# Optimization experiments

Measured on AMD Instinct MI355X. Metric: run time of the kernel, lower is better.

The kernel has to match this reference:

```python
import jax, jax.numpy as jnp
import numpy as np

N = 50000
H = 256
EPS = 1e-5

def setup_inputs() -> dict:
    key = jax.random.key(0)
    ks = jax.random.split(key, 8)
    d = 128
    inp = {
        'x': jax.random.normal(ks[0], (N, d), jnp.float32),
        'edge_index': jax.random.randint(ks[1], (2, 800000), 0, N, jnp.int64),
        'W1': jax.random.normal(ks[2], (d, H), jnp.float32) * (2.0 / d) ** 0.5,
        'b1': jnp.zeros((H,), jnp.float32),
        'g1': jnp.ones((H,), jnp.float32),
        'be1': jnp.zeros((H,), jnp.float32),
        'W2': jax.random.normal(ks[3], (H, H), jnp.float32) * (2.0 / H) ** 0.5,
        'b2': jnp.zeros((H,), jnp.float32),
        'g2': jnp.ones((H,), jnp.float32),
        'be2': jnp.zeros((H,), jnp.float32),
        'W3': jax.random.normal(ks[4], (H, H), jnp.float32) * (2.0 / H) ** 0.5,
        'b3': jnp.zeros((H,), jnp.float32),
        'g3': jnp.ones((H,), jnp.float32),
        'be3': jnp.zeros((H,), jnp.float32),
        'Wf1': jax.random.normal(ks[5], (H, H // 2), jnp.float32) * (2.0 / H) ** 0.5,
        'bf1': jnp.zeros((H // 2,), jnp.float32),
        'Wf2': jax.random.normal(ks[6], (H // 2, 1), jnp.float32) * (2.0 / (H // 2)) ** 0.5,
        'bf2': jnp.zeros((1,), jnp.float32),
    }
    return inp

def _gcn_norm(edge_index):
    # add self-loops, symmetric normalization (PyG GCNConv defaults)
    loop = jnp.arange(N, dtype=edge_index.dtype)
    row = jnp.concatenate([edge_index[0], loop])  # source
    col = jnp.concatenate([edge_index[1], loop])  # target
    deg = jax.ops.segment_sum(jnp.ones_like(col, jnp.float32), col, num_segments=N)
    dis = jnp.where(deg > 0, jax.lax.rsqrt(deg), 0.0)
    norm = dis[row] * dis[col]  # [E+N]
    return row, col, norm

def _conv(x, W, b, row, col, norm):
    xw = x @ W                       # [N,H]
    msg = xw[row] * norm[:, None]    # gather + scale, [E+N,H]
    out = jax.ops.segment_sum(msg, col, num_segments=N)
    return out + b

def _ln(x, g, b):
    mu = jnp.mean(x, axis=-1, keepdims=True)
    var = jnp.var(x, axis=-1, keepdims=True)
    return (x - mu) * jax.lax.rsqrt(var + EPS) * g + b

def reference(x, edge_index, W1, b1, g1, be1, W2, b2, g2, be2, W3, b3, g3, be3, Wf1, bf1, Wf2, bf2):
    row, col, norm = _gcn_norm(edge_index)
    x1 = jax.nn.relu(_ln(_conv(x, W1, b1, row, col, norm), g1, be1))
    x2 = jax.nn.relu(_ln(_conv(x1, W2, b2, row, col, norm), g2, be2)) + 0.7 * x1
    x3 = jax.nn.relu(_ln(_conv(x2, W3, b3, row, col, norm), g3, be3)) * 0.7 + x2
    h = jax.nn.relu(x3 @ Wf1 + bf1)
    return h @ Wf2 + bf2  # [N,1]
```

## Files before the change

kernel.cpp:

```cpp
#include <hip/hip_runtime.h>
#include <cstdint>
#include <cstddef>

#define HDIM 256
#define DIN 128
#define EPSV 1e-5f
#define SCHUNK 1024

typedef __attribute__((ext_vector_type(8))) short short8;
typedef __attribute__((ext_vector_type(4))) float f32x4;

__device__ __forceinline__ float bf2f(unsigned int u16) {
  union { unsigned int i; float f; } v; v.i = u16 << 16; return v.f;
}
__device__ __forceinline__ unsigned short f2bf(float f) {
  union { float f; unsigned int i; } v; v.f = f;
  unsigned int u = v.i;
  return (unsigned short)((u + 0x7fffu + ((u >> 16) & 1u)) >> 16);
}
__device__ __forceinline__ float4 ldbf4(const unsigned short* p) {
  uint2 v = *(const uint2*)p;
  return make_float4(bf2f(v.x & 0xffffu), bf2f(v.x >> 16),
                     bf2f(v.y & 0xffffu), bf2f(v.y >> 16));
}
__device__ __forceinline__ void stbf4(unsigned short* p, float a, float b, float c, float d) {
  uint2 o;
  o.x = (unsigned int)f2bf(a) | ((unsigned int)f2bf(b) << 16);
  o.y = (unsigned int)f2bf(c) | ((unsigned int)f2bf(d) << 16);
  *(uint2*)p = o;
}
#define ACC8(u) do { \
    acc[0] += bf2f((u).x & 0xffffu); acc[1] += bf2f((u).x >> 16); \
    acc[2] += bf2f((u).y & 0xffffu); acc[3] += bf2f((u).y >> 16); \
    acc[4] += bf2f((u).z & 0xffffu); acc[5] += bf2f((u).z >> 16); \
    acc[6] += bf2f((u).w & 0xffffu); acc[7] += bf2f((u).w >> 16); } while (0)

__global__ __launch_bounds__(256) void zero_i_k(int* deg, int* cur, int n) {
  int i = blockIdx.x * 256 + threadIdx.x;
  if (i < n) { deg[i] = 0; cur[i] = 0; }
}

__global__ __launch_bounds__(256) void hist_k(const int* __restrict__ col, int* deg, int e) {
  int i = blockIdx.x * 256 + threadIdx.x;
  if (i < e) atomicAdd(&deg[col[i]], 1);
}

__global__ __launch_bounds__(256) void scanA_k(const int* __restrict__ deg,
                                               int* __restrict__ row_ptr,
                                               int* __restrict__ blockSums,
                                               float* __restrict__ dis, int n) {
  __shared__ int waveSums[4];
  const int tid = threadIdx.x, lane = tid & 63, w = tid >> 6;
  const int base = blockIdx.x * SCHUNK + tid * 4;
  int v0 = 0, v1 = 0, v2 = 0, v3 = 0;
  if (base + 0 < n) v0 = deg[base + 0];
  if (base + 1 < n) v1 = deg[base + 1];
  if (base + 2 < n) v2 = deg[base + 2];
  if (base + 3 < n) v3 = deg[base + 3];
  if (base + 0 < n) dis[base + 0] = rsqrtf((float)(v0 + 1));
  if (base + 1 < n) dis[base + 1] = rsqrtf((float)(v1 + 1));
  if (base + 2 < n) dis[base + 2] = rsqrtf((float)(v2 + 1));
  if (base + 3 < n) dis[base + 3] = rsqrtf((float)(v3 + 1));
  int tsum = v0 + v1 + v2 + v3;
  int inc = tsum;
#pragma unroll
  for (int off = 1; off < 64; off <<= 1) {
    int t = __shfl_up(inc, off);
    if (lane >= off) inc += t;
  }
  if (lane == 63) waveSums[w] = inc;
  __syncthreads();
  int woff = 0;
#pragma unroll
  for (int k = 0; k < 4; ++k) woff += (k < w) ? waveSums[k] : 0;
  int excl = woff + inc - tsum;
  if (base + 0 < n) row_ptr[base + 0] = excl;
  if (base + 1 < n) row_ptr[base + 1] = excl + v0;
  if (base + 2 < n) row_ptr[base + 2] = excl + v0 + v1;
  if (base + 3 < n) row_ptr[base + 3] = excl + v0 + v1 + v2;
  if (tid == 255) blockSums[blockIdx.x] = woff + inc;
}

__global__ __launch_bounds__(256) void scanB_k(int* blockSums, int nb) {
  __shared__ int waveSums[4];
  const int tid = threadIdx.x, lane = tid & 63, w = tid >> 6;
  int v = (tid < nb) ? blockSums[tid] : 0;
  int inc = v;
#pragma unroll
  for (int off = 1; off < 64; off <<= 1) {
    int t = __shfl_up(inc, off);
    if (lane >= off) inc += t;
  }
  if (lane == 63) waveSums[w] = inc;
  __syncthreads();
  int woff = 0;
#pragma unroll
  for (int k = 0; k < 4; ++k) woff += (k < w) ? waveSums[k] : 0;
  if (tid < nb) blockSums[tid] = woff + inc - v;
}

__global__ __launch_bounds__(256) void scanC_k(int* __restrict__ row_ptr,
                                               const int* __restrict__ blockSums,
                                               int n, int e) {
  const int base = blockIdx.x * SCHUNK + threadIdx.x * 4;
  const int add = blockSums[blockIdx.x];
#pragma unroll
  for (int k = 0; k < 4; ++k)
    if (base + k < n) row_ptr[base + k] += add;
  if (blockIdx.x == 0 && threadIdx.x == 0) row_ptr[n] = e;
}

__global__ __launch_bounds__(256) void fill_k(const int* __restrict__ row,
                                              const int* __restrict__ col,
                                              const int* __restrict__ row_ptr,
                                              int* cur, int* srcs, int e) {
  int i = blockIdx.x * 256 + threadIdx.x;
  if (i < e) {
    int c = col[i];
    int p = row_ptr[c] + atomicAdd(&cur[c], 1);
    srcs[p] = row[i];
  }
}

__device__ __forceinline__ void packW(const float* __restrict__ W,
                                      unsigned short* __restrict__ out,
                                      int idx, int C) {
  int j = idx & 7, lane = (idx >> 3) & 63, rest = idx >> 9;
  int NSUB = C >> 4;
  int ns = rest % NSUB, kb = rest / NSUB;
  int k = kb * 32 + (lane >> 4) * 8 + j;
  int c = ns * 16 + (lane & 15);
  out[idx] = f2bf(W[(size_t)k * C + c]);
}

__global__ __launch_bounds__(256) void prep_k(
    const float* __restrict__ W1, const float* __restrict__ W2,
    const float* __restrict__ W3, const float* __restrict__ Wf1,
    const float* __restrict__ x, const float* __restrict__ dis,
    unsigned short* __restrict__ W1p, unsigned short* __restrict__ W2p,
    unsigned short* __restrict__ W3p, unsigned short* __restrict__ Wf1p,
    unsigned short* __restrict__ xs, int nx) {
  int idx = blockIdx.x * 256 + threadIdx.x;
  const int s0 = DIN * HDIM, s1 = s0 + HDIM * HDIM, s2 = s1 + HDIM * HDIM,
            s3 = s2 + HDIM * 128;
  if (idx < s0) packW(W1, W1p, idx, HDIM);
  else if (idx < s1) packW(W2, W2p, idx - s0, HDIM);
  else if (idx < s2) packW(W3, W3p, idx - s1, HDIM);
  else if (idx < s3) packW(Wf1, Wf1p, idx - s2, 128);
  else {
    int o = idx - s3;
    if (o < nx) xs[o] = f2bf(x[o] * dis[o >> 7]);
  }
}

__global__ __launch_bounds__(256) void gather256_k(
    const unsigned short* __restrict__ xs, const int* __restrict__ row_ptr,
    const int* __restrict__ srcs, const float* __restrict__ dis,
    unsigned short* __restrict__ out, int n) {
  int wv = blockIdx.x * 4 + (threadIdx.x >> 6);
  int lane = threadIdx.x & 63;
  int half = lane >> 5, li = lane & 31;
  int i = wv * 2 + half;
  bool valid = i < n;
  int ic = valid ? i : n - 1;
  int beg = row_ptr[ic], end = row_ptr[ic + 1];
  float di = dis[ic];
  const int co = li * 8;
  const unsigned short* xb = xs + co;
  float acc[8];
  {
    uint4 v = *(const uint4*)(xb + (size_t)ic * 256);
    acc[0] = bf2f(v.x & 0xffffu); acc[1] = bf2f(v.x >> 16);
    acc[2] = bf2f(v.y & 0xffffu); acc[3] = bf2f(v.y >> 16);
    acc[4] = bf2f(v.z & 0xffffu); acc[5] = bf2f(v.z >> 16);
    acc[6] = bf2f(v.w & 0xffffu); acc[7] = bf2f(v.w >> 16);
  }
  int j = beg;
  int4 sA, sB;
  if (j + 8 <= end) { sA = *(const int4*)(srcs + j); sB = *(const int4*)(srcs + j + 4); }
  for (; j + 8 <= end;) {
    int4 cA = sA, cB = sB;
    j += 8;
    if (j + 8 <= end) { sA = *(const int4*)(srcs + j); sB = *(const int4*)(srcs + j + 4); }
    uint4 u0 = *(const uint4*)(xb + (size_t)cA.x * 256);
    uint4 u1 = *(const uint4*)(xb + (size_t)cA.y * 256);
    uint4 u2 = *(const uint4*)(xb + (size_t)cA.z * 256);
    uint4 u3 = *(const uint4*)(xb + (size_t)cA.w * 256);
    uint4 u4 = *(const uint4*)(xb + (size_t)cB.x * 256);
    uint4 u5 = *(const uint4*)(xb + (size_t)cB.y * 256);
    uint4 u6 = *(const uint4*)(xb + (size_t)cB.z * 256);
    uint4 u7 = *(const uint4*)(xb + (size_t)cB.w * 256);
    ACC8(u0); ACC8(u1); ACC8(u2); ACC8(u3);
    ACC8(u4); ACC8(u5); ACC8(u6); ACC8(u7);
  }
  for (; j < end; ++j) {
    uint4 u = *(const uint4*)(xb + (size_t)srcs[j] * 256);
    ACC8(u);
  }
  if (valid) {
    uint4 o;
    o.x = (unsigned int)f2bf(di * acc[0]) | ((unsigned int)f2bf(di * acc[1]) << 16);
    o.y = (unsigned int)f2bf(di * acc[2]) | ((unsigned int)f2bf(di * acc[3]) << 16);
    o.z = (unsigned int)f2bf(di * acc[4]) | ((unsigned int)f2bf(di * acc[5]) << 16);
    o.w = (unsigned int)f2bf(di * acc[6]) | ((unsigned int)f2bf(di * acc[7]) << 16);
    *(uint4*)(out + (size_t)i * 256 + co) = o;
  }
}

__global__ __launch_bounds__(256) void gather128_k(
    const unsigned short* __restrict__ xs, const int* __restrict__ row_ptr,
    const int* __restrict__ srcs, const float* __restrict__ dis,
    unsigned short* __restrict__ out, int n) {
  int wv = blockIdx.x * 4 + (threadIdx.x >> 6);
  int lane = threadIdx.x & 63;
  int q = lane >> 4, li = lane & 15;
  int i = wv * 4 + q;
  bool valid = i < n;
  int ic = valid ? i : n - 1;
  int beg = row_ptr[ic], end = row_ptr[ic + 1];
  float di = dis[ic];
  const int co = li * 8;
  const unsigned short* xb = xs + co;
  float acc[8];
  {
    uint4 v = *(const uint4*)(xb + (size_t)ic * 128);
    acc[0] = bf2f(v.x & 0xffffu); acc[1] = bf2f(v.x >> 16);
    acc[2] = bf2f(v.y & 0xffffu); acc[3] = bf2f(v.y >> 16);
    acc[4] = bf2f(v.z & 0xffffu); acc[5] = bf2f(v.z >> 16);
    acc[6] = bf2f(v.w & 0xffffu); acc[7] = bf2f(v.w >> 16);
  }
  int j = beg;
  int4 sA, sB;
  if (j + 8 <= end) { sA = *(const int4*)(srcs + j); sB = *(const int4*)(srcs + j + 4); }
  for (; j + 8 <= end;) {
    int4 cA = sA, cB = sB;
    j += 8;
    if (j + 8 <= end) { sA = *(const int4*)(srcs + j); sB = *(const int4*)(srcs + j + 4); }
    uint4 u0 = *(const uint4*)(xb + (size_t)cA.x * 128);
    uint4 u1 = *(const uint4*)(xb + (size_t)cA.y * 128);
    uint4 u2 = *(const uint4*)(xb + (size_t)cA.z * 128);
    uint4 u3 = *(const uint4*)(xb + (size_t)cA.w * 128);
    uint4 u4 = *(const uint4*)(xb + (size_t)cB.x * 128);
    uint4 u5 = *(const uint4*)(xb + (size_t)cB.y * 128);
    uint4 u6 = *(const uint4*)(xb + (size_t)cB.z * 128);
    uint4 u7 = *(const uint4*)(xb + (size_t)cB.w * 128);
    ACC8(u0); ACC8(u1); ACC8(u2); ACC8(u3);
    ACC8(u4); ACC8(u5); ACC8(u6); ACC8(u7);
  }
  for (; j < end; ++j) {
    uint4 u = *(const uint4*)(xb + (size_t)srcs[j] * 128);
    ACC8(u);
  }
  if (valid) {
    uint4 o;
    o.x = (unsigned int)f2bf(di * acc[0]) | ((unsigned int)f2bf(di * acc[1]) << 16);
    o.y = (unsigned int)f2bf(di * acc[2]) | ((unsigned int)f2bf(di * acc[3]) << 16);
    o.z = (unsigned int)f2bf(di * acc[4]) | ((unsigned int)f2bf(di * acc[5]) << 16);
    o.w = (unsigned int)f2bf(di * acc[6]) | ((unsigned int)f2bf(di * acc[7]) << 16);
    *(uint4*)(out + (size_t)i * 128 + co) = o;
  }
}

template<int MODE, int K>
__global__ __launch_bounds__(512) void gemmln_k(
    const unsigned short* __restrict__ A, const unsigned short* __restrict__ Wp,
    const float* __restrict__ bias, const float* __restrict__ gam,
    const float* __restrict__ bet, const unsigned short* __restrict__ xprev,
    const float* __restrict__ dis, unsigned short* __restrict__ out,
    unsigned short* __restrict__ outs, int n) {
  constexpr int CN = 256, NSUB = 16, KC = K / 32;
  __shared__ float red_s[64][4], red_q[64][4];
  const int t = threadIdx.x;
  const int w = t >> 6, lane = t & 63;
  const int rg = w & 1, cg = w >> 1;
  const int gq = lane >> 4, i = lane & 15;
  const int m0 = blockIdx.x * 64;
  const int r0 = m0 + rg * 32 + i, r1 = r0 + 16;
  const int l0 = r0 < n ? r0 : n - 1, l1 = r1 < n ? r1 : n - 1;
  const unsigned short* a0 = A + (size_t)l0 * K + gq * 8;
  const unsigned short* a1 = A + (size_t)l1 * K + gq * 8;
  const short8* wp = (const short8*)Wp + (size_t)(cg * 4) * 64 + lane;

  f32x4 acc[2][4];
#pragma unroll
  for (int rr = 0; rr < 2; ++rr)
#pragma unroll
    for (int j = 0; j < 4; ++j) acc[rr][j] = (f32x4){0.f, 0.f, 0.f, 0.f};

  short8 af0 = *(const short8*)a0;
  short8 af1 = *(const short8*)a1;
  short8 wf[4];
#pragma unroll
  for (int j = 0; j < 4; ++j) wf[j] = wp[j * 64];

#pragma unroll
  for (int kc = 0; kc < KC; ++kc) {
    short8 naf0, naf1, nwf[4];
    if (kc + 1 < KC) {
      naf0 = *(const short8*)(a0 + (kc + 1) * 32);
      naf1 = *(const short8*)(a1 + (kc + 1) * 32);
#pragma unroll
      for (int j = 0; j < 4; ++j) nwf[j] = wp[(size_t)(kc + 1) * NSUB * 64 + j * 64];
    }
#pragma unroll
    for (int j = 0; j < 4; ++j) {
      acc[0][j] = __builtin_amdgcn_mfma_f32_16x16x32_bf16(wf[j], af0, acc[0][j], 0, 0, 0);
      acc[1][j] = __builtin_amdgcn_mfma_f32_16x16x32_bf16(wf[j], af1, acc[1][j], 0, 0, 0);
    }
    if (kc + 1 < KC) {
      af0 = naf0; af1 = naf1;
#pragma unroll
      for (int j = 0; j < 4; ++j) wf[j] = nwf[j];
    }
  }

  const int colb = cg * 64 + gq * 4;
  float s0 = 0.f, q0 = 0.f, s1 = 0.f, q1 = 0.f;
#pragma unroll
  for (int j = 0; j < 4; ++j) {
    f32x4 b4 = *(const f32x4*)(bias + colb + j * 16);
#pragma unroll
    for (int r = 0; r < 4; ++r) {
      acc[0][j][r] += b4[r];
      acc[1][j][r] += b4[r];
      float v = acc[0][j][r]; s0 += v; q0 += v * v;
      float u = acc[1][j][r]; s1 += u; q1 += u * u;
    }
  }
  s0 += __shfl_xor(s0, 16); s0 += __shfl_xor(s0, 32);
  q0 += __shfl_xor(q0, 16); q0 += __shfl_xor(q0, 32);
  s1 += __shfl_xor(s1, 16); s1 += __shfl_xor(s1, 32);
  q1 += __shfl_xor(q1, 16); q1 += __shfl_xor(q1, 32);
  if (gq == 0) {
    red_s[rg * 32 + i][cg] = s0;      red_q[rg * 32 + i][cg] = q0;
    red_s[rg * 32 + 16 + i][cg] = s1; red_q[rg * 32 + 16 + i][cg] = q1;
  }
  __syncthreads();

#pragma unroll
  for (int rr = 0; rr < 2; ++rr) {
    int il = rg * 32 + rr * 16 + i;
    int r = m0 + il;
    if (r >= n) continue;
    float ss = (red_s[il][0] + red_s[il][1]) + (red_s[il][2] + red_s[il][3]);
    float qq = (red_q[il][0] + red_q[il][1]) + (red_q[il][2] + red_q[il][3]);
    float mu = ss * (1.f / CN);
    float inv = rsqrtf(qq * (1.f / CN) - mu * mu + EPSV);
    float sdi = outs ? dis[r] : 0.f;
    unsigned short* op = out + (size_t)r * CN + colb;
    unsigned short* osp = outs ? outs + (size_t)r * CN + colb : nullptr;
    const unsigned short* pp = (MODE != 0) ? (xprev + (size_t)r * CN + colb) : nullptr;
#pragma unroll
    for (int j = 0; j < 4; ++j) {
      f32x4 g4 = *(const f32x4*)(gam + colb + j * 16);
      f32x4 e4 = *(const f32x4*)(bet + colb + j * 16);
      float o0 = fmaxf((acc[rr][j][0] - mu) * inv * g4[0] + e4[0], 0.f);
      float o1 = fmaxf((acc[rr][j][1] - mu) * inv * g4[1] + e4[1], 0.f);
      float o2 = fmaxf((acc[rr][j][2] - mu) * inv * g4[2] + e4[2], 0.f);
      float o3 = fmaxf((acc[rr][j][3] - mu) * inv * g4[3] + e4[3], 0.f);
      if (MODE == 1) {
        float4 pv = ldbf4(pp + j * 16);
        o0 += 0.7f * pv.x; o1 += 0.7f * pv.y; o2 += 0.7f * pv.z; o3 += 0.7f * pv.w;
      } else if (MODE == 2) {
        float4 pv = ldbf4(pp + j * 16);
        o0 = o0 * 0.7f + pv.x; o1 = o1 * 0.7f + pv.y;
        o2 = o2 * 0.7f + pv.z; o3 = o3 * 0.7f + pv.w;
      }
      stbf4(op + j * 16, o0, o1, o2, o3);
      if (outs) stbf4(osp + j * 16, o0 * sdi, o1 * sdi, o2 * sdi, o3 * sdi);
    }
  }
}

__global__ __launch_bounds__(256) void gemmdot_k(
    const unsigned short* __restrict__ A, const unsigned short* __restrict__ Wp,
    const float* __restrict__ b1, const float* __restrict__ w2,
    const float* __restrict__ b2, float* __restrict__ out, int n) {
  constexpr int K = 256, NSUB = 8, KC = 8;
  __shared__ float redh[64][2];
  const int t = threadIdx.x;
  const int w = t >> 6, lane = t & 63;
  const int rg = w & 1, cg = w >> 1;
  const int gq = lane >> 4, i = lane & 15;
  const int m0 = blockIdx.x * 64;
  const int r0 = m0 + rg * 32 + i, r1 = r0 + 16;
  const int l0 = r0 < n ? r0 : n - 1, l1 = r1 < n ? r1 : n - 1;
  const unsigned short* a0 = A + (size_t)l0 * K + gq * 8;
  const unsigned short* a1 = A + (size_t)l1 * K + gq * 8;
  const short8* wp = (const short8*)Wp + (size_t)(cg * 4) * 64 + lane;

  f32x4 acc[2][4];
#pragma unroll
  for (int rr = 0; rr < 2; ++rr)
#pragma unroll
    for (int j = 0; j < 4; ++j) acc[rr][j] = (f32x4){0.f, 0.f, 0.f, 0.f};

  short8 af0 = *(const short8*)a0;
  short8 af1 = *(const short8*)a1;
  short8 wf[4];
#pragma unroll
  for (int j = 0; j < 4; ++j) wf[j] = wp[j * 64];

#pragma unroll
  for (int kc = 0; kc < KC; ++kc) {
    short8 naf0, naf1, nwf[4];
    if (kc + 1 < KC) {
      naf0 = *(const short8*)(a0 + (kc + 1) * 32);
      naf1 = *(const short8*)(a1 + (kc + 1) * 32);
#pragma unroll
      for (int j = 0; j < 4; ++j) nwf[j] = wp[(size_t)(kc + 1) * NSUB * 64 + j * 64];
    }
#pragma unroll
    for (int j = 0; j < 4; ++j) {
      acc[0][j] = __builtin_amdgcn_mfma_f32_16x16x32_bf16(wf[j], af0, acc[0][j], 0, 0, 0);
      acc[1][j] = __builtin_amdgcn_mfma_f32_16x16x32_bf16(wf[j], af1, acc[1][j], 0, 0, 0);
    }
    if (kc + 1 < KC) {
      af0 = naf0; af1 = naf1;
#pragma unroll
      for (int j = 0; j < 4; ++j) wf[j] = nwf[j];
    }
  }

  const int colb = cg * 64 + gq * 4;
  float p0 = 0.f, p1 = 0.f;
#pragma unroll
  for (int j = 0; j < 4; ++j) {
    f32x4 bb = *(const f32x4*)(b1 + colb + j * 16);
    f32x4 ww = *(const f32x4*)(w2 + colb + j * 16);
#pragma unroll
    for (int r = 0; r < 4; ++r) {
      p0 += fmaxf(acc[0][j][r] + bb[r], 0.f) * ww[r];
      p1 += fmaxf(acc[1][j][r] + bb[r], 0.f) * ww[r];
    }
  }
  p0 += __shfl_xor(p0, 16); p0 += __shfl_xor(p0, 32);
  p1 += __shfl_xor(p1, 16); p1 += __shfl_xor(p1, 32);
  if (gq == 0) {
    redh[rg * 32 + i][cg] = p0;
    redh[rg * 32 + 16 + i][cg] = p1;
  }
  __syncthreads();
  if (t < 64) {
    int r = m0 + t;
    if (r < n) out[r] = redh[t][0] + redh[t][1] + b2[0];
  }
}

extern "C" void kernel_launch(void* const* d_in, const int* in_sizes, int n_in,
                              void* d_out, int out_size, void* d_ws, size_t ws_size,
                              hipStream_t stream) {
  const float* x   = (const float*)d_in[0];
  const int*   ei  = (const int*)d_in[1];
  const float* W1  = (const float*)d_in[2];
  const float* b1  = (const float*)d_in[3];
  const float* g1  = (const float*)d_in[4];
  const float* be1 = (const float*)d_in[5];
  const float* W2  = (const float*)d_in[6];
  const float* b2  = (const float*)d_in[7];
  const float* g2  = (const float*)d_in[8];
  const float* be2 = (const float*)d_in[9];
  const float* W3  = (const float*)d_in[10];
  const float* b3  = (const float*)d_in[11];
  const float* g3  = (const float*)d_in[12];
  const float* be3 = (const float*)d_in[13];
  const float* Wf1 = (const float*)d_in[14];
  const float* bf1 = (const float*)d_in[15];
  const float* Wf2 = (const float*)d_in[16];
  const float* bf2 = (const float*)d_in[17];
  float* out = (float*)d_out;

  const int n = in_sizes[0] / DIN;
  const int e = in_sizes[1] / 2;
  const int* row = ei;
  const int* col = ei + e;

  char* ws = (char*)d_ws;
  size_t off = 0;
  auto alloc = [&](size_t bytes) -> void* {
    void* p = ws + off;
    off = (off + bytes + 255) & ~(size_t)255;
    return p;
  };
  float*          dis     = (float*)alloc((size_t)n * 4);
  int*            deg_i   = (int*)alloc((size_t)n * 4);
  int*            cur     = (int*)alloc((size_t)n * 4);
  int*            row_ptr = (int*)alloc((size_t)(n + 1) * 4);
  int*            bsums   = (int*)alloc((size_t)256 * 4);
  int*            srcs    = (int*)alloc((size_t)e * 4);
  unsigned short* W1p     = (unsigned short*)alloc((size_t)DIN * HDIM * 2);
  unsigned short* W2p     = (unsigned short*)alloc((size_t)HDIM * HDIM * 2);
  unsigned short* W3p     = (unsigned short*)alloc((size_t)HDIM * HDIM * 2);
  unsigned short* Wf1p    = (unsigned short*)alloc((size_t)HDIM * 128 * 2);
  unsigned short* xsb     = (unsigned short*)alloc((size_t)n * DIN * 2);
  unsigned short* agg     = (unsigned short*)alloc((size_t)n * HDIM * 2);
  unsigned short* x1      = (unsigned short*)alloc((size_t)n * HDIM * 2);
  unsigned short* x1s     = (unsigned short*)alloc((size_t)n * HDIM * 2);
  unsigned short* x2      = (unsigned short*)alloc((size_t)n * HDIM * 2);
  unsigned short* x2s     = (unsigned short*)alloc((size_t)n * HDIM * 2);
  unsigned short* a1      = agg;
  unsigned short* x3      = x1;

  const int nb  = (n + 255) / 256;
  const int eb  = (e + 255) / 256;
  const int gb  = (n + 63) / 64;
  const int sb_ = (n + SCHUNK - 1) / SCHUNK;
  const int g2b = (n + 7) / 8;
  const int g1b = (n + 15) / 16;
  const int prep_tot = DIN * HDIM + HDIM * HDIM + HDIM * HDIM + HDIM * 128 + n * DIN;

  zero_i_k<<<nb, 256, 0, stream>>>(deg_i, cur, n);
  hist_k<<<eb, 256, 0, stream>>>(col, deg_i, e);
  scanA_k<<<sb_, 256, 0, stream>>>(deg_i, row_ptr, bsums, dis, n);
  scanB_k<<<1, 256, 0, stream>>>(bsums, sb_);
  scanC_k<<<sb_, 256, 0, stream>>>(row_ptr, bsums, n, e);
  fill_k<<<eb, 256, 0, stream>>>(row, col, row_ptr, cur, srcs, e);

  prep_k<<<(prep_tot + 255) / 256, 256, 0, stream>>>(W1, W2, W3, Wf1, x, dis,
                                                     W1p, W2p, W3p, Wf1p, xsb, n * DIN);

  gather128_k<<<g1b, 256, 0, stream>>>(xsb, row_ptr, srcs, dis, a1, n);
  gemmln_k<0, DIN><<<gb, 512, 0, stream>>>(a1, W1p, b1, g1, be1, nullptr, dis, x1, x1s, n);

  gather256_k<<<g2b, 256, 0, stream>>>(x1s, row_ptr, srcs, dis, agg, n);
  gemmln_k<1, HDIM><<<gb, 512, 0, stream>>>(agg, W2p, b2, g2, be2, x1, dis, x2, x2s, n);

  gather256_k<<<g2b, 256, 0, stream>>>(x2s, row_ptr, srcs, dis, agg, n);
  gemmln_k<2, HDIM><<<gb, 512, 0, stream>>>(agg, W3p, b3, g3, be3, x2, dis, x3, nullptr, n);

  gemmdot_k<<<gb, 256, 0, stream>>>(x3, Wf1p, bf1, Wf2, bf2, out, n);
}
```

Baseline: 484.6 us.

## Store only scaled activations, merge scan passes, widen gather unroll, memset counters

The layer-norm GEMMs now write only the dis-scaled activation and recover the unscaled residual by multiplying with 1/dis. This drops one full N×256 bf16 store per layer and the separate residual buffers. The block-sum scan kernel is folded into scanC, where each block reduces its preceding block sums. The zeroing kernel is replaced by a single hipMemsetAsync. The gather loops issue 16 independent row loads per iteration instead of software-pipelining 8. The residual path now takes an extra bf16 rounding and a division by dis, which adds a small accuracy risk.

```diff
diff --git a/kernel.cpp b/kernel.cpp
--- a/kernel.cpp
+++ b/kernel.cpp
@@ -34,11 +34,6 @@
     acc[2] += bf2f((u).y & 0xffffu); acc[3] += bf2f((u).y >> 16); \
     acc[4] += bf2f((u).z & 0xffffu); acc[5] += bf2f((u).z >> 16); \
     acc[6] += bf2f((u).w & 0xffffu); acc[7] += bf2f((u).w >> 16); } while (0)
-
-__global__ __launch_bounds__(256) void zero_i_k(int* deg, int* cur, int n) {
-  int i = blockIdx.x * 256 + threadIdx.x;
-  if (i < n) { deg[i] = 0; cur[i] = 0; }
-}
 
 __global__ __launch_bounds__(256) void hist_k(const int* __restrict__ col, int* deg, int e) {
   int i = blockIdx.x * 256 + threadIdx.x;
@@ -81,29 +76,19 @@
   if (tid == 255) blockSums[blockIdx.x] = woff + inc;
 }
 
-__global__ __launch_bounds__(256) void scanB_k(int* blockSums, int nb) {
-  __shared__ int waveSums[4];
-  const int tid = threadIdx.x, lane = tid & 63, w = tid >> 6;
-  int v = (tid < nb) ? blockSums[tid] : 0;
-  int inc = v;
-#pragma unroll
-  for (int off = 1; off < 64; off <<= 1) {
-    int t = __shfl_up(inc, off);
-    if (lane >= off) inc += t;
-  }
-  if (lane == 63) waveSums[w] = inc;
+__global__ __launch_bounds__(256) void scanC_k(int* __restrict__ row_ptr,
+                                               const int* __restrict__ bsums,
+                                               int n, int e, int nbs) {
+  __shared__ int s_add;
+  if (threadIdx.x < 64) {
+    int v = (threadIdx.x < nbs && threadIdx.x < blockIdx.x) ? bsums[threadIdx.x] : 0;
+#pragma unroll
+    for (int off = 1; off < 64; off <<= 1) v += __shfl_xor(v, off);
+    if (threadIdx.x == 0) s_add = v;
+  }
   __syncthreads();
-  int woff = 0;
-#pragma unroll
-  for (int k = 0; k < 4; ++k) woff += (k < w) ? waveSums[k] : 0;
-  if (tid < nb) blockSums[tid] = woff + inc - v;
-}
-
-__global__ __launch_bounds__(256) void scanC_k(int* __restrict__ row_ptr,
-                                               const int* __restrict__ blockSums,
-                                               int n, int e) {
+  const int add = s_add;
   const int base = blockIdx.x * SCHUNK + threadIdx.x * 4;
-  const int add = blockSums[blockIdx.x];
 #pragma unroll
   for (int k = 0; k < 4; ++k)
     if (base + k < n) row_ptr[base + k] += add;
@@ -176,22 +161,39 @@
     acc[6] = bf2f(v.w & 0xffffu); acc[7] = bf2f(v.w >> 16);
   }
   int j = beg;
-  int4 sA, sB;
-  if (j + 8 <= end) { sA = *(const int4*)(srcs + j); sB = *(const int4*)(srcs + j + 4); }
-  for (; j + 8 <= end;) {
-    int4 cA = sA, cB = sB;
-    j += 8;
-    if (j + 8 <= end) { sA = *(const int4*)(srcs + j); sB = *(const int4*)(srcs + j + 4); }
-    uint4 u0 = *(const uint4*)(xb + (size_t)cA.x * 256);
-    uint4 u1 = *(const uint4*)(xb + (size_t)cA.y * 256);
-    uint4 u2 = *(const uint4*)(xb + (size_t)cA.z * 256);
-    uint4 u3 = *(const uint4*)(xb + (size_t)cA.w * 256);
-    uint4 u4 = *(const uint4*)(xb + (size_t)cB.x * 256);
-    uint4 u5 = *(const uint4*)(xb + (size_t)cB.y * 256);
-    uint4 u6 = *(const uint4*)(xb + (size_t)cB.z * 256);
-    uint4 u7 = *(const uint4*)(xb + (size_t)cB.w * 256);
+  for (; j + 16 <= end; j += 16) {
+    int4 sA = *(const int4*)(srcs + j);
+    int4 sB = *(const int4*)(srcs + j + 4);
+    int4 sC = *(const int4*)(srcs + j + 8);
+    int4 sD = *(const int4*)(srcs + j + 12);
+    uint4 u0 = *(const uint4*)(xb + (size_t)sA.x * 256);
+    uint4 u1 = *(const uint4*)(xb + (size_t)sA.y * 256);
+    uint4 u2 = *(const uint4*)(xb + (size_t)sA.z * 256);
+    uint4 u3 = *(const uint4*)(xb + (size_t)sA.w * 256);
+    uint4 u4 = *(const uint4*)(xb + (size_t)sB.x * 256);
+    uint4 u5 = *(const uint4*)(xb + (size_t)sB.y * 256);
+    uint4 u6 = *(const uint4*)(xb + (size_t)sB.z * 256);
+    uint4 u7 = *(const uint4*)(xb + (size_t)sB.w * 256);
+    uint4 u8 = *(const uint4*)(xb + (size_t)sC.x * 256);
+    uint4 u9 = *(const uint4*)(xb + (size_t)sC.y * 256);
+    uint4 uA = *(const uint4*)(xb + (size_t)sC.z * 256);
+    uint4 uB = *(const uint4*)(xb + (size_t)sC.w * 256);
+    uint4 uC = *(const uint4*)(xb + (size_t)sD.x * 256);
+    uint4 uD = *(const uint4*)(xb + (size_t)sD.y * 256);
+    uint4 uE = *(const uint4*)(xb + (size_t)sD.z * 256);
+    uint4 uF = *(const uint4*)(xb + (size_t)sD.w * 256);
     ACC8(u0); ACC8(u1); ACC8(u2); ACC8(u3);
     ACC8(u4); ACC8(u5); ACC8(u6); ACC8(u7);
+    ACC8(u8); ACC8(u9); ACC8(uA); ACC8(uB);
+    ACC8(uC); ACC8(uD); ACC8(uE); ACC8(uF);
+  }
+  for (; j + 4 <= end; j += 4) {
+    int4 sA = *(const int4*)(srcs + j);
+    uint4 u0 = *(const uint4*)(xb + (size_t)sA.x * 256);
+    uint4 u1 = *(const uint4*)(xb + (size_t)sA.y * 256);
+    uint4 u2 = *(const uint4*)(xb + (size_t)sA.z * 256);
+    uint4 u3 = *(const uint4*)(xb + (size_t)sA.w * 256);
+    ACC8(u0); ACC8(u1); ACC8(u2); ACC8(u3);
   }
   for (; j < end; ++j) {
     uint4 u = *(const uint4*)(xb + (size_t)srcs[j] * 256);
@@ -230,22 +232,39 @@
     acc[6] = bf2f(v.w & 0xffffu); acc[7] = bf2f(v.w >> 16);
   }
   int j = beg;
-  int4 sA, sB;
-  if (j + 8 <= end) { sA = *(const int4*)(srcs + j); sB = *(const int4*)(srcs + j + 4); }
-  for (; j + 8 <= end;) {
-    int4 cA = sA, cB = sB;
-    j += 8;
-    if (j + 8 <= end) { sA = *(const int4*)(srcs + j); sB = *(const int4*)(srcs + j + 4); }
-    uint4 u0 = *(const uint4*)(xb + (size_t)cA.x * 128);
-    uint4 u1 = *(const uint4*)(xb + (size_t)cA.y * 128);
-    uint4 u2 = *(const uint4*)(xb + (size_t)cA.z * 128);
-    uint4 u3 = *(const uint4*)(xb + (size_t)cA.w * 128);
-    uint4 u4 = *(const uint4*)(xb + (size_t)cB.x * 128);
-    uint4 u5 = *(const uint4*)(xb + (size_t)cB.y * 128);
-    uint4 u6 = *(const uint4*)(xb + (size_t)cB.z * 128);
-    uint4 u7 = *(const uint4*)(xb + (size_t)cB.w * 128);
+  for (; j + 16 <= end; j += 16) {
+    int4 sA = *(const int4*)(srcs + j);
+    int4 sB = *(const int4*)(srcs + j + 4);
+    int4 sC = *(const int4*)(srcs + j + 8);
+    int4 sD = *(const int4*)(srcs + j + 12);
+    uint4 u0 = *(const uint4*)(xb + (size_t)sA.x * 128);
+    uint4 u1 = *(const uint4*)(xb + (size_t)sA.y * 128);
+    uint4 u2 = *(const uint4*)(xb + (size_t)sA.z * 128);
+    uint4 u3 = *(const uint4*)(xb + (size_t)sA.w * 128);
+    uint4 u4 = *(const uint4*)(xb + (size_t)sB.x * 128);
+    uint4 u5 = *(const uint4*)(xb + (size_t)sB.y * 128);
+    uint4 u6 = *(const uint4*)(xb + (size_t)sB.z * 128);
+    uint4 u7 = *(const uint4*)(xb + (size_t)sB.w * 128);
+    uint4 u8 = *(const uint4*)(xb + (size_t)sC.x * 128);
+    uint4 u9 = *(const uint4*)(xb + (size_t)sC.y * 128);
+    uint4 uA = *(const uint4*)(xb + (size_t)sC.z * 128);
+    uint4 uB = *(const uint4*)(xb + (size_t)sC.w * 128);
+    uint4 uC = *(const uint4*)(xb + (size_t)sD.x * 128);
+    uint4 uD = *(const uint4*)(xb + (size_t)sD.y * 128);
+    uint4 uE = *(const uint4*)(xb + (size_t)sD.z * 128);
+    uint4 uF = *(const uint4*)(xb + (size_t)sD.w * 128);
     ACC8(u0); ACC8(u1); ACC8(u2); ACC8(u3);
     ACC8(u4); ACC8(u5); ACC8(u6); ACC8(u7);
+    ACC8(u8); ACC8(u9); ACC8(uA); ACC8(uB);
+    ACC8(uC); ACC8(uD); ACC8(uE); ACC8(uF);
+  }
+  for (; j + 4 <= end; j += 4) {
+    int4 sA = *(const int4*)(srcs + j);
+    uint4 u0 = *(const uint4*)(xb + (size_t)sA.x * 128);
+    uint4 u1 = *(const uint4*)(xb + (size_t)sA.y * 128);
+    uint4 u2 = *(const uint4*)(xb + (size_t)sA.z * 128);
+    uint4 u3 = *(const uint4*)(xb + (size_t)sA.w * 128);
+    ACC8(u0); ACC8(u1); ACC8(u2); ACC8(u3);
   }
   for (; j < end; ++j) {
     uint4 u = *(const uint4*)(xb + (size_t)srcs[j] * 128);
@@ -261,13 +280,12 @@
   }
 }
 
-template<int MODE, int K>
+template<int MODE, int K, bool SOUT>
 __global__ __launch_bounds__(512) void gemmln_k(
     const unsigned short* __restrict__ A, const unsigned short* __restrict__ Wp,
     const float* __restrict__ bias, const float* __restrict__ gam,
     const float* __restrict__ bet, const unsigned short* __restrict__ xprev,
-    const float* __restrict__ dis, unsigned short* __restrict__ out,
-    unsigned short* __restrict__ outs, int n) {
+    const float* __restrict__ dis, unsigned short* __restrict__ out, int n) {
   constexpr int CN = 256, NSUB = 16, KC = K / 32;
   __shared__ float red_s[64][4], red_q[64][4];
   const int t = threadIdx.x;
@@ -346,9 +364,9 @@
     float qq = (red_q[il][0] + red_q[il][1]) + (red_q[il][2] + red_q[il][3]);
     float mu = ss * (1.f / CN);
     float inv = rsqrtf(qq * (1.f / CN) - mu * mu + EPSV);
-    float sdi = outs ? dis[r] : 0.f;
+    float di = dis[r];
+    float rinv = (MODE != 0) ? 1.0f / di : 0.f;
     unsigned short* op = out + (size_t)r * CN + colb;
-    unsigned short* osp = outs ? outs + (size_t)r * CN + colb : nullptr;
     const unsigned short* pp = (MODE != 0) ? (xprev + (size_t)r * CN + colb) : nullptr;
 #pragma unroll
     for (int j = 0; j < 4; ++j) {
@@ -360,14 +378,15 @@
       float o3 = fmaxf((acc[rr][j][3] - mu) * inv * g4[3] + e4[3], 0.f);
       if (MODE == 1) {
         float4 pv = ldbf4(pp + j * 16);
-        o0 += 0.7f * pv.x; o1 += 0.7f * pv.y; o2 += 0.7f * pv.z; o3 += 0.7f * pv.w;
+        o0 += 0.7f * rinv * pv.x; o1 += 0.7f * rinv * pv.y;
+        o2 += 0.7f * rinv * pv.z; o3 += 0.7f * rinv * pv.w;
       } else if (MODE == 2) {
         float4 pv = ldbf4(pp + j * 16);
-        o0 = o0 * 0.7f + pv.x; o1 = o1 * 0.7f + pv.y;
-        o2 = o2 * 0.7f + pv.z; o3 = o3 * 0.7f + pv.w;
+        o0 = o0 * 0.7f + rinv * pv.x; o1 = o1 * 0.7f + rinv * pv.y;
+        o2 = o2 * 0.7f + rinv * pv.z; o3 = o3 * 0.7f + rinv * pv.w;
       }
+      if (SOUT) { o0 *= di; o1 *= di; o2 *= di; o3 *= di; }
       stbf4(op + j * 16, o0, o1, o2, o3);
-      if (outs) stbf4(osp + j * 16, o0 * sdi, o1 * sdi, o2 * sdi, o3 * sdi);
     }
   }
 }
@@ -494,14 +513,11 @@
   unsigned short* Wf1p    = (unsigned short*)alloc((size_t)HDIM * 128 * 2);
   unsigned short* xsb     = (unsigned short*)alloc((size_t)n * DIN * 2);
   unsigned short* agg     = (unsigned short*)alloc((size_t)n * HDIM * 2);
-  unsigned short* x1      = (unsigned short*)alloc((size_t)n * HDIM * 2);
   unsigned short* x1s     = (unsigned short*)alloc((size_t)n * HDIM * 2);
-  unsigned short* x2      = (unsigned short*)alloc((size_t)n * HDIM * 2);
   unsigned short* x2s     = (unsigned short*)alloc((size_t)n * HDIM * 2);
   unsigned short* a1      = agg;
-  unsigned short* x3      = x1;
-
-  const int nb  = (n + 255) / 256;
+  unsigned short* x3      = x1s;
+
   const int eb  = (e + 255) / 256;
   const int gb  = (n + 63) / 64;
   const int sb_ = (n + SCHUNK - 1) / SCHUNK;
@@ -509,24 +525,23 @@
   const int g1b = (n + 15) / 16;
   const int prep_tot = DIN * HDIM + HDIM * HDIM + HDIM * HDIM + HDIM * 128 + n * DIN;
 
-  zero_i_k<<<nb, 256, 0, stream>>>(deg_i, cur, n);
+  hipMemsetAsync(deg_i, 0, ((char*)row_ptr - (char*)deg_i), stream);
   hist_k<<<eb, 256, 0, stream>>>(col, deg_i, e);
   scanA_k<<<sb_, 256, 0, stream>>>(deg_i, row_ptr, bsums, dis, n);
-  scanB_k<<<1, 256, 0, stream>>>(bsums, sb_);
-  scanC_k<<<sb_, 256, 0, stream>>>(row_ptr, bsums, n, e);
+  scanC_k<<<sb_, 256, 0, stream>>>(row_ptr, bsums, n, e, sb_);
   fill_k<<<eb, 256, 0, stream>>>(row, col, row_ptr, cur, srcs, e);
 
   prep_k<<<(prep_tot + 255) / 256, 256, 0, stream>>>(W1, W2, W3, Wf1, x, dis,
                                                      W1p, W2p, W3p, Wf1p, xsb, n * DIN);
 
   gather128_k<<<g1b, 256, 0, stream>>>(xsb, row_ptr, srcs, dis, a1, n);
-  gemmln_k<0, DIN><<<gb, 512, 0, stream>>>(a1, W1p, b1, g1, be1, nullptr, dis, x1, x1s, n);
+  gemmln_k<0, DIN, true><<<gb, 512, 0, stream>>>(a1, W1p, b1, g1, be1, nullptr, dis, x1s, n);
 
   gather256_k<<<g2b, 256, 0, stream>>>(x1s, row_ptr, srcs, dis, agg, n);
-  gemmln_k<1, HDIM><<<gb, 512, 0, stream>>>(agg, W2p, b2, g2, be2, x1, dis, x2, x2s, n);
+  gemmln_k<1, HDIM, true><<<gb, 512, 0, stream>>>(agg, W2p, b2, g2, be2, x1s, dis, x2s, n);
 
   gather256_k<<<g2b, 256, 0, stream>>>(x2s, row_ptr, srcs, dis, agg, n);
-  gemmln_k<2, HDIM><<<gb, 512, 0, stream>>>(agg, W3p, b3, g3, be3, x2, dis, x3, nullptr, n);
+  gemmln_k<2, HDIM, false><<<gb, 512, 0, stream>>>(agg, W3p, b3, g3, be3, x2s, dis, x3, n);
 
   gemmdot_k<<<gb, 256, 0, stream>>>(x3, Wf1p, bf1, Wf2, bf2, out, n);
 }
```

After: 470.5 us. 1.03x faster.
